# Kernel optimization log

Measured on AMD Instinct MI355X. Metric: run time of the kernel, lower is better.

## Reference

```python
import jax, jax.numpy as jnp
import numpy as np

N, A, C = 4096, 512, 100


def setup_inputs() -> dict:
    key = jax.random.key(0)
    k1, k2, k3 = jax.random.split(key, 3)
    features = jax.random.normal(k1, (N, A), dtype=jnp.float32)
    y_s = jax.random.normal(k2, (N, C), dtype=jnp.float32)
    labels = jax.random.randint(k3, (N,), 0, C, dtype=jnp.int64)
    CoVariance = jnp.zeros((C, A, A), dtype=jnp.float32)
    Ave = jnp.zeros((C, A), dtype=jnp.float32)
    Amount = jnp.zeros((C,), dtype=jnp.float32)
    return {"features": features, "y_s": y_s, "CoVariance": CoVariance,
            "Ave": Ave, "Amount": Amount, "labels": labels}


def reference(features, y_s, CoVariance, Ave, Amount, labels):
    n, a = features.shape
    c = Ave.shape[0]
    dt = features.dtype

    onehot = jax.nn.one_hot(labels, c, dtype=dt)            # [N, C]
    counts = onehot.sum(axis=0)                             # [C]
    counts_safe = jnp.where(counts == 0, 1.0, counts)       # Amount_CxA==0 -> 1

    # per-class mean: ave_CxA [C, A]
    sum_feats = onehot.T @ features                          # [C, A]
    ave_CxA = sum_feats / counts_safe[:, None]

    # centered features w.r.t. own-class mean; masked per-class copies
    centered = features - ave_CxA[labels]                    # [N, A]
    masked = onehot.T[:, :, None] * centered[None, :, :]     # [C, N, A]
    # per-class scatter of outer products (equals torch bmm over zero-padded rows)
    var_temp = jnp.einsum('cna,nb->cab', masked, centered) / counts_safe[:, None, None]

    # mixing weights; NaN (0/0) -> 0
    denom = counts + Amount                                  # [C]
    w = jnp.where(denom > 0, counts / denom, 0.0)            # [C]

    ave_old = jax.lax.stop_gradient(Ave)                     # .detach() in torch
    cov_old = jax.lax.stop_gradient(CoVariance)
    diff = ave_old - ave_CxA                                 # [C, A]
    additional_CV = (w * (1.0 - w))[:, None, None] * jnp.einsum('ca,cb->cab', diff, diff)

    new_cov = cov_old * (1.0 - w)[:, None, None] + var_temp * w[:, None, None] + additional_CV
    new_ave = ave_old * (1.0 - w)[:, None] + ave_CxA * w[:, None]
    new_amount = Amount + counts

    logp = jax.nn.log_softmax(y_s, axis=-1)                  # [N, C]
    loss = -jnp.mean(jnp.take_along_axis(logp, labels[:, None], axis=1))

    return loss, new_cov, new_ave, new_amount
```

## Files before the change

### kernel.cpp

```cpp
#include <hip/hip_runtime.h>


#define TM 128
#define KC 16
#define LSTR 132

__global__ void fused_prep(const int* __restrict__ labels, const float* __restrict__ Amount,
                           int* __restrict__ offsets, int* __restrict__ cursors,
                           float* __restrict__ w_arr, float* __restrict__ inv_cs,
                           float* __restrict__ amount_out, float* __restrict__ loss_acc,
                           int N, int C) {
    __shared__ int hist[1024];
    __shared__ int offs[1025];
    int tid = threadIdx.x;
    for (int c = tid; c < C; c += blockDim.x) hist[c] = 0;
    __syncthreads();
    for (int i = tid; i < N; i += blockDim.x) atomicAdd(&hist[labels[i]], 1);
    __syncthreads();
    if (tid == 0) {
        int o = 0;
        for (int c = 0; c < C; ++c) { offs[c] = o; o += hist[c]; }
        offs[C] = o;
    }
    __syncthreads();
    for (int c = tid; c < C; c += blockDim.x) {
        float cf = (float)hist[c];
        float cs = cf > 0.f ? cf : 1.f;
        inv_cs[c] = 1.f / cs;
        float am = Amount[c];
        float dn = cf + am;
        w_arr[c] = dn > 0.f ? cf / dn : 0.f;
        amount_out[c] = am + cf;
        offsets[c] = offs[c];
        cursors[c] = 0;
    }
    if (tid == 0) { offsets[C] = offs[C]; loss_acc[0] = 0.f; }
}

__global__ void scatter_kernel(const int* __restrict__ labels, const int* __restrict__ offsets,
                               int* __restrict__ cursors, int* __restrict__ idx_sorted, int N) {
    int n = blockIdx.x * blockDim.x + threadIdx.x;
    if (n < N) {
        int c = labels[n];
        int pos = atomicAdd(&cursors[c], 1);
        idx_sorted[offsets[c] + pos] = n;
    }
}

__global__ __launch_bounds__(128) void ave_kernel(
    const float* __restrict__ feats, const float* __restrict__ Ave_in,
    const int* __restrict__ idx_sorted, const int* __restrict__ offsets,
    const float* __restrict__ w_arr, const float* __restrict__ inv_cs,
    float* __restrict__ ave_new, float* __restrict__ ave_out, int A) {
    __shared__ int idxs[512];
    const int c = blockIdx.y;
    const int col = blockIdx.x * 128 + threadIdx.x;
    const int base = offsets[c];
    const int nc = offsets[c + 1] - base;
    float sum = 0.f;
    for (int i0 = 0; i0 < nc; i0 += 512) {
        int chunk = min(512, nc - i0);
        __syncthreads();
        for (int j = threadIdx.x; j < chunk; j += 128) idxs[j] = idx_sorted[base + i0 + j];
        __syncthreads();
        int j = 0;
        for (; j + 3 < chunk; j += 4) {
            int r0 = idxs[j], r1 = idxs[j + 1], r2 = idxs[j + 2], r3 = idxs[j + 3];
            float f0 = feats[(size_t)r0 * A + col];
            float f1 = feats[(size_t)r1 * A + col];
            float f2 = feats[(size_t)r2 * A + col];
            float f3 = feats[(size_t)r3 * A + col];
            sum += f0 + f1 + f2 + f3;
        }
        for (; j < chunk; ++j) sum += feats[(size_t)idxs[j] * A + col];
    }
    float av = sum * inv_cs[c];
    ave_new[(size_t)c * A + col] = av;
    float w = w_arr[c];
    ave_out[(size_t)c * A + col] = Ave_in[(size_t)c * A + col] * (1.f - w) + av * w;
}

__global__ __launch_bounds__(256) void cov_kernel(
    const float* __restrict__ feats, const float* __restrict__ cov_in,
    const float* __restrict__ ave_new, const float* __restrict__ Ave_in,
    const int* __restrict__ idx_sorted, const int* __restrict__ offsets,
    const float* __restrict__ w_arr, const float* __restrict__ inv_cs,
    float* __restrict__ cov_out, int A) {
    const int c  = blockIdx.z;
    const int a0 = blockIdx.y * TM;
    const int b0 = blockIdx.x * TM;
    const int tid = threadIdx.x;
    const int ty = tid >> 4, tx = tid & 15;

    __shared__ float Xa[KC][LSTR];
    __shared__ float Xb[KC][LSTR];
    __shared__ float aveA[TM], aveB[TM], dA[TM], dB[TM];

    if (tid < TM) {
        float av = ave_new[(size_t)c * A + a0 + tid];
        aveA[tid] = av;
        dA[tid] = Ave_in[(size_t)c * A + a0 + tid] - av;
    } else {
        int t = tid - TM;
        float bv = ave_new[(size_t)c * A + b0 + t];
        aveB[t] = bv;
        dB[t] = Ave_in[(size_t)c * A + b0 + t] - bv;
    }

    const float w   = w_arr[c];
    const float omw = 1.f - w;
    const float s   = inv_cs[c] * w;
    const float aw  = w * omw;
    const size_t cbase = (size_t)c * A * A;

    float acc[2][4][2][4] = {};

    if (s > 0.f) {
        if (omw != 0.f) {
            const float sc = omw / s;
            #pragma unroll
            for (int ri = 0; ri < 2; ++ri)
                #pragma unroll
                for (int i = 0; i < 4; ++i) {
                    const size_t rowo = cbase + (size_t)(a0 + ri * 64 + ty * 4 + i) * A + b0;
                    #pragma unroll
                    for (int ci = 0; ci < 2; ++ci) {
                        float4 co = *reinterpret_cast<const float4*>(&cov_in[rowo + ci * 64 + tx * 4]);
                        acc[ri][i][ci][0] = co.x * sc;
                        acc[ri][i][ci][1] = co.y * sc;
                        acc[ri][i][ci][2] = co.z * sc;
                        acc[ri][i][ci][3] = co.w * sc;
                    }
                }
        }

        const int base = offsets[c];
        const int nc = offsets[c + 1] - base;
        const int li = ty;
        const int cg = tx * 4;

        __syncthreads();

        for (int kk = 0; kk < nc; kk += KC) {
            const int kn = min(KC, nc - kk);
            float4 va0 = make_float4(0.f, 0.f, 0.f, 0.f), va1 = va0, vb0 = va0, vb1 = va0;
            if (li < kn) {
                int row = idx_sorted[base + kk + li];
                const float* fr = feats + (size_t)row * A;
                va0 = *reinterpret_cast<const float4*>(fr + a0 + cg);
                va1 = *reinterpret_cast<const float4*>(fr + a0 + cg + 64);
                vb0 = *reinterpret_cast<const float4*>(fr + b0 + cg);
                vb1 = *reinterpret_cast<const float4*>(fr + b0 + cg + 64);
                va0.x -= aveA[cg];      va0.y -= aveA[cg + 1];      va0.z -= aveA[cg + 2];      va0.w -= aveA[cg + 3];
                va1.x -= aveA[cg + 64]; va1.y -= aveA[cg + 65];     va1.z -= aveA[cg + 66];     va1.w -= aveA[cg + 67];
                vb0.x -= aveB[cg];      vb0.y -= aveB[cg + 1];      vb0.z -= aveB[cg + 2];      vb0.w -= aveB[cg + 3];
                vb1.x -= aveB[cg + 64]; vb1.y -= aveB[cg + 65];     vb1.z -= aveB[cg + 66];     vb1.w -= aveB[cg + 67];
            }
            __syncthreads();
            *reinterpret_cast<float4*>(&Xa[li][cg])      = va0;
            *reinterpret_cast<float4*>(&Xa[li][cg + 64]) = va1;
            *reinterpret_cast<float4*>(&Xb[li][cg])      = vb0;
            *reinterpret_cast<float4*>(&Xb[li][cg + 64]) = vb1;
            __syncthreads();

            #pragma unroll
            for (int k = 0; k < KC; ++k) {
                float4 a0v = *reinterpret_cast<const float4*>(&Xa[k][ty * 4]);
                float4 a1v = *reinterpret_cast<const float4*>(&Xa[k][64 + ty * 4]);
                float4 b0v = *reinterpret_cast<const float4*>(&Xb[k][tx * 4]);
                float4 b1v = *reinterpret_cast<const float4*>(&Xb[k][64 + tx * 4]);
                float af[2][4] = {{a0v.x, a0v.y, a0v.z, a0v.w}, {a1v.x, a1v.y, a1v.z, a1v.w}};
                float bf[2][4] = {{b0v.x, b0v.y, b0v.z, b0v.w}, {b1v.x, b1v.y, b1v.z, b1v.w}};
                #pragma unroll
                for (int ri = 0; ri < 2; ++ri)
                    #pragma unroll
                    for (int i = 0; i < 4; ++i)
                        #pragma unroll
                        for (int ci = 0; ci < 2; ++ci)
                            #pragma unroll
                            for (int j = 0; j < 4; ++j)
                                acc[ri][i][ci][j] += af[ri][i] * bf[ci][j];
            }
        }

        float db[2][4];
        #pragma unroll
        for (int ci = 0; ci < 2; ++ci)
            #pragma unroll
            for (int j = 0; j < 4; ++j) db[ci][j] = dB[ci * 64 + tx * 4 + j];

        #pragma unroll
        for (int ri = 0; ri < 2; ++ri)
            #pragma unroll
            for (int i = 0; i < 4; ++i) {
                float da = dA[ri * 64 + ty * 4 + i];
                const size_t rowo = cbase + (size_t)(a0 + ri * 64 + ty * 4 + i) * A + b0;
                #pragma unroll
                for (int ci = 0; ci < 2; ++ci) {
                    float4 res;
                    res.x = acc[ri][i][ci][0] * s + aw * da * db[ci][0];
                    res.y = acc[ri][i][ci][1] * s + aw * da * db[ci][1];
                    res.z = acc[ri][i][ci][2] * s + aw * da * db[ci][2];
                    res.w = acc[ri][i][ci][3] * s + aw * da * db[ci][3];
                    *reinterpret_cast<float4*>(&cov_out[rowo + ci * 64 + tx * 4]) = res;
                }
            }
    } else {
        #pragma unroll
        for (int ri = 0; ri < 2; ++ri)
            #pragma unroll
            for (int i = 0; i < 4; ++i) {
                const size_t rowo = cbase + (size_t)(a0 + ri * 64 + ty * 4 + i) * A + b0;
                #pragma unroll
                for (int ci = 0; ci < 2; ++ci) {
                    float4 co = *reinterpret_cast<const float4*>(&cov_in[rowo + ci * 64 + tx * 4]);
                    float4 res = make_float4(co.x * omw, co.y * omw, co.z * omw, co.w * omw);
                    *reinterpret_cast<float4*>(&cov_out[rowo + ci * 64 + tx * 4]) = res;
                }
            }
    }
}

__global__ __launch_bounds__(256) void loss_kernel(
    const float* __restrict__ y_s, const int* __restrict__ labels,
    float* __restrict__ loss_acc, int N, int C) {
    __shared__ float bsum[4];
    const int lane = threadIdx.x & 63;
    const int wv = threadIdx.x >> 6;
    const int gw = blockIdx.x * 4 + wv;
    const int nwaves = gridDim.x * 4;
    float wsum = 0.f;
    for (int r = gw; r < N; r += nwaves) {
        const float* row = y_s + (size_t)r * C;
        float m = -1e30f;
        for (int col = lane; col < C; col += 64) m = fmaxf(m, row[col]);
        #pragma unroll
        for (int off = 32; off > 0; off >>= 1) m = fmaxf(m, __shfl_xor(m, off));
        float se = 0.f;
        for (int col = lane; col < C; col += 64) se += __expf(row[col] - m);
        #pragma unroll
        for (int off = 32; off > 0; off >>= 1) se += __shfl_xor(se, off);
        if (lane == 0) wsum += -(row[labels[r]] - m - __logf(se));
    }
    if (lane == 0) bsum[wv] = wsum;
    __syncthreads();
    if (threadIdx.x == 0) {
        float t = bsum[0] + bsum[1] + bsum[2] + bsum[3];
        atomicAdd(loss_acc, t);
    }
}

__global__ void finalize_kernel(const float* __restrict__ loss_acc, float* __restrict__ out_loss,
                                float invN) {
    if (threadIdx.x == 0 && blockIdx.x == 0) out_loss[0] = loss_acc[0] * invN;
}

extern "C" void kernel_launch(void* const* d_in, const int* in_sizes, int n_in,
                              void* d_out, int out_size, void* d_ws, size_t ws_size,
                              hipStream_t stream) {
    const float* feats  = (const float*)d_in[0];
    const float* y_s    = (const float*)d_in[1];
    const float* cov_in = (const float*)d_in[2];
    const float* Ave_in = (const float*)d_in[3];
    const float* Amount = (const float*)d_in[4];
    const int*   labels = (const int*)d_in[5];

    const int C = in_sizes[4];
    const int N = in_sizes[5];
    const int A = in_sizes[3] / C;

    float* out      = (float*)d_out;
    float* out_loss = out;
    float* out_cov  = out + 1;
    float* out_ave  = out_cov + (size_t)C * A * A;
    float* out_amt  = out_ave + (size_t)C * A;

    char* w8 = (char*)d_ws;
    int* offsets    = (int*)w8;   w8 += (size_t)(C + 1) * sizeof(int);
    int* cursors    = (int*)w8;   w8 += (size_t)C * sizeof(int);
    int* idx_sorted = (int*)w8;   w8 += (size_t)N * sizeof(int);
    float* loss_acc = (float*)w8; w8 += sizeof(float);
    float* w_arr    = (float*)w8; w8 += (size_t)C * sizeof(float);
    float* inv_cs   = (float*)w8; w8 += (size_t)C * sizeof(float);
    float* ave_new  = (float*)w8; w8 += (size_t)C * A * sizeof(float);

    fused_prep<<<1, 1024, 0, stream>>>(labels, Amount, offsets, cursors, w_arr, inv_cs,
                                       out_amt, loss_acc, N, C);
    scatter_kernel<<<(N + 255) / 256, 256, 0, stream>>>(labels, offsets, cursors, idx_sorted, N);
    ave_kernel<<<dim3(A / 128, C), 128, 0, stream>>>(feats, Ave_in, idx_sorted, offsets,
                                                     w_arr, inv_cs, ave_new, out_ave, A);
    dim3 grid(A / TM, A / TM, C);
    cov_kernel<<<grid, 256, 0, stream>>>(feats, cov_in, ave_new, Ave_in, idx_sorted, offsets,
                                         w_arr, inv_cs, out_cov, A);
    loss_kernel<<<64, 256, 0, stream>>>(y_s, labels, loss_acc, N, C);
    finalize_kernel<<<1, 64, 0, stream>>>(loss_acc, out_loss, 1.f / (float)N);
}
```

Baseline: 263.6 us.

## Use bf16 MFMA for per-class covariance and fuse prep/scatter/finalize kernels

Moves the per-class covariance outer-product accumulation from FP32 FMA tiles to bf16 MFMA 16x16x32 instructions. Centered features are rounded to bf16 and staged transposed in LDS, with a K-chunk of 32. The scatter of sorted indices is folded into the single-block prep kernel using LDS cursors, and the loss finalize kernel is removed by pre-scaling the atomic adds. Together these cut FP32 ALU cost and launch overhead, but they reduce precision of the covariance and use scalar, less-coalesced global stores in the MFMA output layout.

After: 270.4 us. +2.6%, slower.

```diff
diff --git a/kernel.cpp b/kernel.cpp
--- a/kernel.cpp
+++ b/kernel.cpp
@@ -2,20 +2,30 @@
 
 
 #define TM 128
-#define KC 16
-#define LSTR 132
-
-__global__ void fused_prep(const int* __restrict__ labels, const float* __restrict__ Amount,
-                           int* __restrict__ offsets, int* __restrict__ cursors,
-                           float* __restrict__ w_arr, float* __restrict__ inv_cs,
-                           float* __restrict__ amount_out, float* __restrict__ loss_acc,
-                           int N, int C) {
+#define KC 32
+#define KCP 40
+
+typedef __attribute__((ext_vector_type(8))) short bf16x8;
+typedef __attribute__((ext_vector_type(4))) float f32x4;
+
+__device__ __forceinline__ unsigned short f2bf(float f) {
+    unsigned u = __float_as_uint(f);
+    u += 0x7fffu + ((u >> 16) & 1u);
+    return (unsigned short)(u >> 16);
+}
+
+__global__ __launch_bounds__(1024) void prep_kernel(
+    const int* __restrict__ labels, const float* __restrict__ Amount,
+    int* __restrict__ offsets, int* __restrict__ idx_sorted,
+    float* __restrict__ w_arr, float* __restrict__ inv_cs,
+    float* __restrict__ amount_out, float* __restrict__ out_loss0, int N, int C) {
     __shared__ int hist[1024];
     __shared__ int offs[1025];
-    int tid = threadIdx.x;
-    for (int c = tid; c < C; c += blockDim.x) hist[c] = 0;
-    __syncthreads();
-    for (int i = tid; i < N; i += blockDim.x) atomicAdd(&hist[labels[i]], 1);
+    __shared__ int cur[1024];
+    const int tid = threadIdx.x;
+    for (int c = tid; c < C; c += 1024) { hist[c] = 0; cur[c] = 0; }
+    __syncthreads();
+    for (int i = tid; i < N; i += 1024) atomicAdd(&hist[labels[i]], 1);
     __syncthreads();
     if (tid == 0) {
         int o = 0;
@@ -23,7 +33,7 @@
         offs[C] = o;
     }
     __syncthreads();
-    for (int c = tid; c < C; c += blockDim.x) {
+    for (int c = tid; c < C; c += 1024) {
         float cf = (float)hist[c];
         float cs = cf > 0.f ? cf : 1.f;
         inv_cs[c] = 1.f / cs;
@@ -32,18 +42,12 @@
         w_arr[c] = dn > 0.f ? cf / dn : 0.f;
         amount_out[c] = am + cf;
         offsets[c] = offs[c];
-        cursors[c] = 0;
-    }
-    if (tid == 0) { offsets[C] = offs[C]; loss_acc[0] = 0.f; }
-}
-
-__global__ void scatter_kernel(const int* __restrict__ labels, const int* __restrict__ offsets,
-                               int* __restrict__ cursors, int* __restrict__ idx_sorted, int N) {
-    int n = blockIdx.x * blockDim.x + threadIdx.x;
-    if (n < N) {
-        int c = labels[n];
-        int pos = atomicAdd(&cursors[c], 1);
-        idx_sorted[offsets[c] + pos] = n;
+    }
+    if (tid == 0) { offsets[C] = offs[C]; out_loss0[0] = 0.f; }
+    for (int i = tid; i < N; i += 1024) {
+        int c = labels[i];
+        int p = atomicAdd(&cur[c], 1);
+        idx_sorted[offs[c] + p] = i;
     }
 }
 
@@ -65,11 +69,10 @@
         __syncthreads();
         int j = 0;
         for (; j + 3 < chunk; j += 4) {
-            int r0 = idxs[j], r1 = idxs[j + 1], r2 = idxs[j + 2], r3 = idxs[j + 3];
-            float f0 = feats[(size_t)r0 * A + col];
-            float f1 = feats[(size_t)r1 * A + col];
-            float f2 = feats[(size_t)r2 * A + col];
-            float f3 = feats[(size_t)r3 * A + col];
+            float f0 = feats[(size_t)idxs[j] * A + col];
+            float f1 = feats[(size_t)idxs[j + 1] * A + col];
+            float f2 = feats[(size_t)idxs[j + 2] * A + col];
+            float f3 = feats[(size_t)idxs[j + 3] * A + col];
             sum += f0 + f1 + f2 + f3;
         }
         for (; j < chunk; ++j) sum += feats[(size_t)idxs[j] * A + col];
@@ -90,22 +93,10 @@
     const int a0 = blockIdx.y * TM;
     const int b0 = blockIdx.x * TM;
     const int tid = threadIdx.x;
-    const int ty = tid >> 4, tx = tid & 15;
-
-    __shared__ float Xa[KC][LSTR];
-    __shared__ float Xb[KC][LSTR];
-    __shared__ float aveA[TM], aveB[TM], dA[TM], dB[TM];
-
-    if (tid < TM) {
-        float av = ave_new[(size_t)c * A + a0 + tid];
-        aveA[tid] = av;
-        dA[tid] = Ave_in[(size_t)c * A + a0 + tid] - av;
-    } else {
-        int t = tid - TM;
-        float bv = ave_new[(size_t)c * A + b0 + t];
-        aveB[t] = bv;
-        dB[t] = Ave_in[(size_t)c * A + b0 + t] - bv;
-    }
+
+    __shared__ __align__(16) unsigned short XT[2][TM][KCP];
+    __shared__ float dA[TM], dB[TM];
+    __shared__ int idx_lds[KC];
 
     const float w   = w_arr[c];
     const float omw = 1.f - w;
@@ -113,117 +104,109 @@
     const float aw  = w * omw;
     const size_t cbase = (size_t)c * A * A;
 
-    float acc[2][4][2][4] = {};
-
     if (s > 0.f) {
+        const int side = tid >> 7;
+        const int col  = tid & 127;
+        const int gcol = (side ? b0 : a0) + col;
+        const float mean = ave_new[(size_t)c * A + gcol];
+        if (side == 0) dA[col] = Ave_in[(size_t)c * A + gcol] - mean;
+        else           dB[col] = Ave_in[(size_t)c * A + gcol] - mean;
+
+        const int wave = tid >> 6;
+        const int qm = wave >> 1, qn = wave & 1;
+        const int lane = tid & 63;
+        const int lq = lane >> 4, lr = lane & 15;
+
+        f32x4 acc[4][4];
         if (omw != 0.f) {
             const float sc = omw / s;
             #pragma unroll
-            for (int ri = 0; ri < 2; ++ri)
-                #pragma unroll
-                for (int i = 0; i < 4; ++i) {
-                    const size_t rowo = cbase + (size_t)(a0 + ri * 64 + ty * 4 + i) * A + b0;
+            for (int i = 0; i < 4; ++i)
+                #pragma unroll
+                for (int j = 0; j < 4; ++j) {
+                    const int n = qn * 64 + j * 16 + lr;
                     #pragma unroll
-                    for (int ci = 0; ci < 2; ++ci) {
-                        float4 co = *reinterpret_cast<const float4*>(&cov_in[rowo + ci * 64 + tx * 4]);
-                        acc[ri][i][ci][0] = co.x * sc;
-                        acc[ri][i][ci][1] = co.y * sc;
-                        acc[ri][i][ci][2] = co.z * sc;
-                        acc[ri][i][ci][3] = co.w * sc;
+                    for (int reg = 0; reg < 4; ++reg) {
+                        const int m = qm * 64 + i * 16 + lq * 4 + reg;
+                        acc[i][j][reg] = cov_in[cbase + (size_t)(a0 + m) * A + b0 + n] * sc;
                     }
                 }
+        } else {
+            #pragma unroll
+            for (int i = 0; i < 4; ++i)
+                #pragma unroll
+                for (int j = 0; j < 4; ++j)
+                    acc[i][j] = (f32x4){0.f, 0.f, 0.f, 0.f};
         }
 
         const int base = offsets[c];
         const int nc = offsets[c + 1] - base;
-        const int li = ty;
-        const int cg = tx * 4;
-
-        __syncthreads();
 
         for (int kk = 0; kk < nc; kk += KC) {
-            const int kn = min(KC, nc - kk);
-            float4 va0 = make_float4(0.f, 0.f, 0.f, 0.f), va1 = va0, vb0 = va0, vb1 = va0;
-            if (li < kn) {
-                int row = idx_sorted[base + kk + li];
-                const float* fr = feats + (size_t)row * A;
-                va0 = *reinterpret_cast<const float4*>(fr + a0 + cg);
-                va1 = *reinterpret_cast<const float4*>(fr + a0 + cg + 64);
-                vb0 = *reinterpret_cast<const float4*>(fr + b0 + cg);
-                vb1 = *reinterpret_cast<const float4*>(fr + b0 + cg + 64);
-                va0.x -= aveA[cg];      va0.y -= aveA[cg + 1];      va0.z -= aveA[cg + 2];      va0.w -= aveA[cg + 3];
-                va1.x -= aveA[cg + 64]; va1.y -= aveA[cg + 65];     va1.z -= aveA[cg + 66];     va1.w -= aveA[cg + 67];
-                vb0.x -= aveB[cg];      vb0.y -= aveB[cg + 1];      vb0.z -= aveB[cg + 2];      vb0.w -= aveB[cg + 3];
-                vb1.x -= aveB[cg + 64]; vb1.y -= aveB[cg + 65];     vb1.z -= aveB[cg + 66];     vb1.w -= aveB[cg + 67];
+            __syncthreads();
+            if (tid < KC) idx_lds[tid] = (kk + tid < nc) ? idx_sorted[base + kk + tid] : 0;
+            __syncthreads();
+            #pragma unroll
+            for (int mg = 0; mg < KC / 4; ++mg) {
+                unsigned short q0, q1, q2, q3;
+                {
+                    int m = mg * 4;
+                    float v0 = (kk + m + 0 < nc) ? feats[(size_t)idx_lds[m + 0] * A + gcol] - mean : 0.f;
+                    float v1 = (kk + m + 1 < nc) ? feats[(size_t)idx_lds[m + 1] * A + gcol] - mean : 0.f;
+                    float v2 = (kk + m + 2 < nc) ? feats[(size_t)idx_lds[m + 2] * A + gcol] - mean : 0.f;
+                    float v3 = (kk + m + 3 < nc) ? feats[(size_t)idx_lds[m + 3] * A + gcol] - mean : 0.f;
+                    q0 = f2bf(v0); q1 = f2bf(v1); q2 = f2bf(v2); q3 = f2bf(v3);
+                }
+                uint2 pk;
+                pk.x = (unsigned)q0 | ((unsigned)q1 << 16);
+                pk.y = (unsigned)q2 | ((unsigned)q3 << 16);
+                *reinterpret_cast<uint2*>(&XT[side][col][mg * 4]) = pk;
             }
             __syncthreads();
-            *reinterpret_cast<float4*>(&Xa[li][cg])      = va0;
-            *reinterpret_cast<float4*>(&Xa[li][cg + 64]) = va1;
-            *reinterpret_cast<float4*>(&Xb[li][cg])      = vb0;
-            *reinterpret_cast<float4*>(&Xb[li][cg + 64]) = vb1;
-            __syncthreads();
-
-            #pragma unroll
-            for (int k = 0; k < KC; ++k) {
-                float4 a0v = *reinterpret_cast<const float4*>(&Xa[k][ty * 4]);
-                float4 a1v = *reinterpret_cast<const float4*>(&Xa[k][64 + ty * 4]);
-                float4 b0v = *reinterpret_cast<const float4*>(&Xb[k][tx * 4]);
-                float4 b1v = *reinterpret_cast<const float4*>(&Xb[k][64 + tx * 4]);
-                float af[2][4] = {{a0v.x, a0v.y, a0v.z, a0v.w}, {a1v.x, a1v.y, a1v.z, a1v.w}};
-                float bf[2][4] = {{b0v.x, b0v.y, b0v.z, b0v.w}, {b1v.x, b1v.y, b1v.z, b1v.w}};
-                #pragma unroll
-                for (int ri = 0; ri < 2; ++ri)
-                    #pragma unroll
-                    for (int i = 0; i < 4; ++i)
-                        #pragma unroll
-                        for (int ci = 0; ci < 2; ++ci)
-                            #pragma unroll
-                            for (int j = 0; j < 4; ++j)
-                                acc[ri][i][ci][j] += af[ri][i] * bf[ci][j];
-            }
-        }
-
-        float db[2][4];
+            bf16x8 af[4], bfr[4];
+            #pragma unroll
+            for (int i = 0; i < 4; ++i)
+                af[i] = *reinterpret_cast<const bf16x8*>(&XT[0][qm * 64 + i * 16 + lr][lq * 8]);
+            #pragma unroll
+            for (int j = 0; j < 4; ++j)
+                bfr[j] = *reinterpret_cast<const bf16x8*>(&XT[1][qn * 64 + j * 16 + lr][lq * 8]);
+            #pragma unroll
+            for (int i = 0; i < 4; ++i)
+                #pragma unroll
+                for (int j = 0; j < 4; ++j)
+                    acc[i][j] = __builtin_amdgcn_mfma_f32_16x16x32_bf16(af[i], bfr[j], acc[i][j], 0, 0, 0);
+        }
+
         #pragma unroll
-        for (int ci = 0; ci < 2; ++ci)
-            #pragma unroll
-            for (int j = 0; j < 4; ++j) db[ci][j] = dB[ci * 64 + tx * 4 + j];
-
-        #pragma unroll
-        for (int ri = 0; ri < 2; ++ri)
-            #pragma unroll
-            for (int i = 0; i < 4; ++i) {
-                float da = dA[ri * 64 + ty * 4 + i];
-                const size_t rowo = cbase + (size_t)(a0 + ri * 64 + ty * 4 + i) * A + b0;
-                #pragma unroll
-                for (int ci = 0; ci < 2; ++ci) {
-                    float4 res;
-                    res.x = acc[ri][i][ci][0] * s + aw * da * db[ci][0];
-                    res.y = acc[ri][i][ci][1] * s + aw * da * db[ci][1];
-                    res.z = acc[ri][i][ci][2] * s + aw * da * db[ci][2];
-                    res.w = acc[ri][i][ci][3] * s + aw * da * db[ci][3];
-                    *reinterpret_cast<float4*>(&cov_out[rowo + ci * 64 + tx * 4]) = res;
+        for (int i = 0; i < 4; ++i) {
+            #pragma unroll
+            for (int reg = 0; reg < 4; ++reg) {
+                const int m = qm * 64 + i * 16 + lq * 4 + reg;
+                const float da = aw * dA[m];
+                float* rowp = cov_out + cbase + (size_t)(a0 + m) * A + b0;
+                #pragma unroll
+                for (int j = 0; j < 4; ++j) {
+                    const int n = qn * 64 + j * 16 + lr;
+                    rowp[n] = acc[i][j][reg] * s + da * dB[n];
                 }
             }
+        }
     } else {
-        #pragma unroll
-        for (int ri = 0; ri < 2; ++ri)
-            #pragma unroll
-            for (int i = 0; i < 4; ++i) {
-                const size_t rowo = cbase + (size_t)(a0 + ri * 64 + ty * 4 + i) * A + b0;
-                #pragma unroll
-                for (int ci = 0; ci < 2; ++ci) {
-                    float4 co = *reinterpret_cast<const float4*>(&cov_in[rowo + ci * 64 + tx * 4]);
-                    float4 res = make_float4(co.x * omw, co.y * omw, co.z * omw, co.w * omw);
-                    *reinterpret_cast<float4*>(&cov_out[rowo + ci * 64 + tx * 4]) = res;
-                }
-            }
+        const float sc = omw;
+        for (int t = tid; t < TM * TM / 4; t += 256) {
+            const int r = t >> 5;
+            const int c4 = (t & 31) * 4;
+            const size_t o = cbase + (size_t)(a0 + r) * A + b0 + c4;
+            float4 co = *reinterpret_cast<const float4*>(&cov_in[o]);
+            float4 res = make_float4(co.x * sc, co.y * sc, co.z * sc, co.w * sc);
+            *reinterpret_cast<float4*>(&cov_out[o]) = res;
+        }
     }
 }
 
 __global__ __launch_bounds__(256) void loss_kernel(
     const float* __restrict__ y_s, const int* __restrict__ labels,
-    float* __restrict__ loss_acc, int N, int C) {
+    float* __restrict__ out_loss0, int N, int C, float invN) {
     __shared__ float bsum[4];
     const int lane = threadIdx.x & 63;
     const int wv = threadIdx.x >> 6;
@@ -245,14 +228,9 @@
     if (lane == 0) bsum[wv] = wsum;
     __syncthreads();
     if (threadIdx.x == 0) {
-        float t = bsum[0] + bsum[1] + bsum[2] + bsum[3];
-        atomicAdd(loss_acc, t);
-    }
-}
-
-__global__ void finalize_kernel(const float* __restrict__ loss_acc, float* __restrict__ out_loss,
-                                float invN) {
-    if (threadIdx.x == 0 && blockIdx.x == 0) out_loss[0] = loss_acc[0] * invN;
+        float t = (bsum[0] + bsum[1] + bsum[2] + bsum[3]) * invN;
+        atomicAdd(out_loss0, t);
+    }
 }
 
 extern "C" void kernel_launch(void* const* d_in, const int* in_sizes, int n_in,
@@ -277,21 +255,17 @@
 
     char* w8 = (char*)d_ws;
     int* offsets    = (int*)w8;   w8 += (size_t)(C + 1) * sizeof(int);
-    int* cursors    = (int*)w8;   w8 += (size_t)C * sizeof(int);
     int* idx_sorted = (int*)w8;   w8 += (size_t)N * sizeof(int);
-    float* loss_acc = (float*)w8; w8 += sizeof(float);
     float* w_arr    = (float*)w8; w8 += (size_t)C * sizeof(float);
     float* inv_cs   = (float*)w8; w8 += (size_t)C * sizeof(float);
     float* ave_new  = (float*)w8; w8 += (size_t)C * A * sizeof(float);
 
-    fused_prep<<<1, 1024, 0, stream>>>(labels, Amount, offsets, cursors, w_arr, inv_cs,
-                                       out_amt, loss_acc, N, C);
-    scatter_kernel<<<(N + 255) / 256, 256, 0, stream>>>(labels, offsets, cursors, idx_sorted, N);
+    prep_kernel<<<1, 1024, 0, stream>>>(labels, Amount, offsets, idx_sorted,
+                                        w_arr, inv_cs, out_amt, out_loss, N, C);
     ave_kernel<<<dim3(A / 128, C), 128, 0, stream>>>(feats, Ave_in, idx_sorted, offsets,
                                                      w_arr, inv_cs, ave_new, out_ave, A);
     dim3 grid(A / TM, A / TM, C);
     cov_kernel<<<grid, 256, 0, stream>>>(feats, cov_in, ave_new, Ave_in, idx_sorted, offsets,
                                          w_arr, inv_cs, out_cov, A);
-    loss_kernel<<<64, 256, 0, stream>>>(y_s, labels, loss_acc, N, C);
-    finalize_kernel<<<1, 64, 0, stream>>>(loss_acc, out_loss, 1.f / (float)N);
-}
+    loss_kernel<<<64, 256, 0, stream>>>(y_s, labels, out_loss, N, C, 1.f / (float)N);
+}
```

## Fuse scatter into prep; fold mean and loss into covariance kernel

Applied to the files above, without the earlier changes.

Moves the label scatter into the single-block prep kernel using shared-memory cursors. The separate per-class mean kernel and the loss and finalize kernels are removed. Each covariance tile block now recomputes its own column means, and an extra z-slice of the grid computes the loss by atomically adding pre-scaled partial sums. This cuts the launch count from six to two and drops the ave_new round trip through memory, at the cost of every tile block re-reading the class rows to build its means, which is redundant work.

Result: slower. 344.0 us (+30.5%).

```diff
diff --git a/kernel.cpp b/kernel.cpp
--- a/kernel.cpp
+++ b/kernel.cpp
@@ -5,17 +5,18 @@
 #define KC 16
 #define LSTR 132
 
-__global__ void fused_prep(const int* __restrict__ labels, const float* __restrict__ Amount,
-                           int* __restrict__ offsets, int* __restrict__ cursors,
-                           float* __restrict__ w_arr, float* __restrict__ inv_cs,
-                           float* __restrict__ amount_out, float* __restrict__ loss_acc,
-                           int N, int C) {
+__global__ __launch_bounds__(1024) void prep_kernel(
+    const int* __restrict__ labels, const float* __restrict__ Amount,
+    int* __restrict__ offsets, int* __restrict__ idx_sorted,
+    float* __restrict__ w_arr, float* __restrict__ inv_cs,
+    float* __restrict__ amount_out, float* __restrict__ out_loss0, int N, int C) {
     __shared__ int hist[1024];
     __shared__ int offs[1025];
-    int tid = threadIdx.x;
-    for (int c = tid; c < C; c += blockDim.x) hist[c] = 0;
-    __syncthreads();
-    for (int i = tid; i < N; i += blockDim.x) atomicAdd(&hist[labels[i]], 1);
+    __shared__ int cur[1024];
+    const int tid = threadIdx.x;
+    for (int c = tid; c < C; c += 1024) { hist[c] = 0; cur[c] = 0; }
+    __syncthreads();
+    for (int i = tid; i < N; i += 1024) atomicAdd(&hist[labels[i]], 1);
     __syncthreads();
     if (tid == 0) {
         int o = 0;
@@ -23,7 +24,7 @@
         offs[C] = o;
     }
     __syncthreads();
-    for (int c = tid; c < C; c += blockDim.x) {
+    for (int c = tid; c < C; c += 1024) {
         float cf = (float)hist[c];
         float cs = cf > 0.f ? cf : 1.f;
         inv_cs[c] = 1.f / cs;
@@ -32,90 +33,94 @@
         w_arr[c] = dn > 0.f ? cf / dn : 0.f;
         amount_out[c] = am + cf;
         offsets[c] = offs[c];
-        cursors[c] = 0;
-    }
-    if (tid == 0) { offsets[C] = offs[C]; loss_acc[0] = 0.f; }
+    }
+    if (tid == 0) { offsets[C] = offs[C]; out_loss0[0] = 0.f; }
+    for (int i = tid; i < N; i += 1024) {
+        int c = labels[i];
+        int p = atomicAdd(&cur[c], 1);
+        idx_sorted[offs[c] + p] = i;
+    }
 }
 
-__global__ void scatter_kernel(const int* __restrict__ labels, const int* __restrict__ offsets,
-                               int* __restrict__ cursors, int* __restrict__ idx_sorted, int N) {
-    int n = blockIdx.x * blockDim.x + threadIdx.x;
-    if (n < N) {
-        int c = labels[n];
-        int pos = atomicAdd(&cursors[c], 1);
-        idx_sorted[offsets[c] + pos] = n;
-    }
-}
-
-__global__ __launch_bounds__(128) void ave_kernel(
-    const float* __restrict__ feats, const float* __restrict__ Ave_in,
-    const int* __restrict__ idx_sorted, const int* __restrict__ offsets,
-    const float* __restrict__ w_arr, const float* __restrict__ inv_cs,
-    float* __restrict__ ave_new, float* __restrict__ ave_out, int A) {
-    __shared__ int idxs[512];
-    const int c = blockIdx.y;
-    const int col = blockIdx.x * 128 + threadIdx.x;
-    const int base = offsets[c];
-    const int nc = offsets[c + 1] - base;
-    float sum = 0.f;
-    for (int i0 = 0; i0 < nc; i0 += 512) {
-        int chunk = min(512, nc - i0);
+__global__ __launch_bounds__(256) void fused_kernel(
+    const float* __restrict__ feats, const float* __restrict__ cov_in,
+    const float* __restrict__ Ave_in, const float* __restrict__ y_s,
+    const int* __restrict__ labels, const int* __restrict__ idx_sorted,
+    const int* __restrict__ offsets, const float* __restrict__ w_arr,
+    const float* __restrict__ inv_cs,
+    float* __restrict__ out_cov, float* __restrict__ out_ave,
+    float* __restrict__ out_loss0, int N, int C, int A, float invN) {
+
+    if ((int)blockIdx.z == C) {
+        __shared__ float bsum[4];
+        const int lane = threadIdx.x & 63;
+        const int wv = threadIdx.x >> 6;
+        const int gw = ((blockIdx.y * gridDim.x + blockIdx.x) << 2) + wv;
+        const int nwaves = gridDim.x * gridDim.y * 4;
+        float wsum = 0.f;
+        for (int r = gw; r < N; r += nwaves) {
+            const float* row = y_s + (size_t)r * C;
+            float m = -1e30f;
+            for (int col = lane; col < C; col += 64) m = fmaxf(m, row[col]);
+            #pragma unroll
+            for (int off = 32; off > 0; off >>= 1) m = fmaxf(m, __shfl_xor(m, off));
+            float se = 0.f;
+            for (int col = lane; col < C; col += 64) se += __expf(row[col] - m);
+            #pragma unroll
+            for (int off = 32; off > 0; off >>= 1) se += __shfl_xor(se, off);
+            if (lane == 0) wsum += -(row[labels[r]] - m - __logf(se));
+        }
+        if (lane == 0) bsum[wv] = wsum;
         __syncthreads();
-        for (int j = threadIdx.x; j < chunk; j += 128) idxs[j] = idx_sorted[base + i0 + j];
-        __syncthreads();
-        int j = 0;
-        for (; j + 3 < chunk; j += 4) {
-            int r0 = idxs[j], r1 = idxs[j + 1], r2 = idxs[j + 2], r3 = idxs[j + 3];
-            float f0 = feats[(size_t)r0 * A + col];
-            float f1 = feats[(size_t)r1 * A + col];
-            float f2 = feats[(size_t)r2 * A + col];
-            float f3 = feats[(size_t)r3 * A + col];
-            sum += f0 + f1 + f2 + f3;
-        }
-        for (; j < chunk; ++j) sum += feats[(size_t)idxs[j] * A + col];
-    }
-    float av = sum * inv_cs[c];
-    ave_new[(size_t)c * A + col] = av;
-    float w = w_arr[c];
-    ave_out[(size_t)c * A + col] = Ave_in[(size_t)c * A + col] * (1.f - w) + av * w;
-}
-
-__global__ __launch_bounds__(256) void cov_kernel(
-    const float* __restrict__ feats, const float* __restrict__ cov_in,
-    const float* __restrict__ ave_new, const float* __restrict__ Ave_in,
-    const int* __restrict__ idx_sorted, const int* __restrict__ offsets,
-    const float* __restrict__ w_arr, const float* __restrict__ inv_cs,
-    float* __restrict__ cov_out, int A) {
+        if (threadIdx.x == 0)
+            atomicAdd(out_loss0, (bsum[0] + bsum[1] + bsum[2] + bsum[3]) * invN);
+        return;
+    }
+
     const int c  = blockIdx.z;
     const int a0 = blockIdx.y * TM;
     const int b0 = blockIdx.x * TM;
     const int tid = threadIdx.x;
-    const int ty = tid >> 4, tx = tid & 15;
 
     __shared__ float Xa[KC][LSTR];
     __shared__ float Xb[KC][LSTR];
     __shared__ float aveA[TM], aveB[TM], dA[TM], dB[TM];
 
-    if (tid < TM) {
-        float av = ave_new[(size_t)c * A + a0 + tid];
-        aveA[tid] = av;
-        dA[tid] = Ave_in[(size_t)c * A + a0 + tid] - av;
-    } else {
-        int t = tid - TM;
-        float bv = ave_new[(size_t)c * A + b0 + t];
-        aveB[t] = bv;
-        dB[t] = Ave_in[(size_t)c * A + b0 + t] - bv;
-    }
-
+    const int base = offsets[c];
+    const int nc = offsets[c + 1] - base;
     const float w   = w_arr[c];
     const float omw = 1.f - w;
     const float s   = inv_cs[c] * w;
     const float aw  = w * omw;
     const size_t cbase = (size_t)c * A * A;
 
-    float acc[2][4][2][4] = {};
+    const int side = tid >> 7;
+    const int col  = tid & 127;
+    const int gcol = (side ? b0 : a0) + col;
+    float sum = 0.f;
+    {
+        int j = 0;
+        for (; j + 3 < nc; j += 4) {
+            int r0 = idx_sorted[base + j];
+            int r1 = idx_sorted[base + j + 1];
+            int r2 = idx_sorted[base + j + 2];
+            int r3 = idx_sorted[base + j + 3];
+            sum += feats[(size_t)r0 * A + gcol] + feats[(size_t)r1 * A + gcol]
+                 + feats[(size_t)r2 * A + gcol] + feats[(size_t)r3 * A + gcol];
+        }
+        for (; j < nc; ++j) sum += feats[(size_t)idx_sorted[base + j] * A + gcol];
+    }
+    const float mean = sum * inv_cs[c];
+    if (side == 0) { aveA[col] = mean; dA[col] = Ave_in[(size_t)c * A + gcol] - mean; }
+    else           { aveB[col] = mean; dB[col] = Ave_in[(size_t)c * A + gcol] - mean; }
+    if (blockIdx.x == 0 && side == 0)
+        out_ave[(size_t)c * A + gcol] = Ave_in[(size_t)c * A + gcol] * omw + mean * w;
+    __syncthreads();
+
+    const int ty = tid >> 4, tx = tid & 15;
 
     if (s > 0.f) {
+        float acc[2][4][2][4] = {};
         if (omw != 0.f) {
             const float sc = omw / s;
             #pragma unroll
@@ -134,12 +139,8 @@
                 }
         }
 
-        const int base = offsets[c];
-        const int nc = offsets[c + 1] - base;
         const int li = ty;
         const int cg = tx * 4;
-
-        __syncthreads();
 
         for (int kk = 0; kk < nc; kk += KC) {
             const int kn = min(KC, nc - kk);
@@ -151,10 +152,10 @@
                 va1 = *reinterpret_cast<const float4*>(fr + a0 + cg + 64);
                 vb0 = *reinterpret_cast<const float4*>(fr + b0 + cg);
                 vb1 = *reinterpret_cast<const float4*>(fr + b0 + cg + 64);
-                va0.x -= aveA[cg];      va0.y -= aveA[cg + 1];      va0.z -= aveA[cg + 2];      va0.w -= aveA[cg + 3];
-                va1.x -= aveA[cg + 64]; va1.y -= aveA[cg + 65];     va1.z -= aveA[cg + 66];     va1.w -= aveA[cg + 67];
-                vb0.x -= aveB[cg];      vb0.y -= aveB[cg + 1];      vb0.z -= aveB[cg + 2];      vb0.w -= aveB[cg + 3];
-                vb1.x -= aveB[cg + 64]; vb1.y -= aveB[cg + 65];     vb1.z -= aveB[cg + 66];     vb1.w -= aveB[cg + 67];
+                va0.x -= aveA[cg];      va0.y -= aveA[cg + 1];  va0.z -= aveA[cg + 2];  va0.w -= aveA[cg + 3];
+                va1.x -= aveA[cg + 64]; va1.y -= aveA[cg + 65]; va1.z -= aveA[cg + 66]; va1.w -= aveA[cg + 67];
+                vb0.x -= aveB[cg];      vb0.y -= aveB[cg + 1];  vb0.z -= aveB[cg + 2];  vb0.w -= aveB[cg + 3];
+                vb1.x -= aveB[cg + 64]; vb1.y -= aveB[cg + 65]; vb1.z -= aveB[cg + 66]; vb1.w -= aveB[cg + 67];
             }
             __syncthreads();
             *reinterpret_cast<float4*>(&Xa[li][cg])      = va0;
@@ -193,66 +194,28 @@
         for (int ri = 0; ri < 2; ++ri)
             #pragma unroll
             for (int i = 0; i < 4; ++i) {
-                float da = dA[ri * 64 + ty * 4 + i];
+                float da = aw * dA[ri * 64 + ty * 4 + i];
                 const size_t rowo = cbase + (size_t)(a0 + ri * 64 + ty * 4 + i) * A + b0;
                 #pragma unroll
                 for (int ci = 0; ci < 2; ++ci) {
                     float4 res;
-                    res.x = acc[ri][i][ci][0] * s + aw * da * db[ci][0];
-                    res.y = acc[ri][i][ci][1] * s + aw * da * db[ci][1];
-                    res.z = acc[ri][i][ci][2] * s + aw * da * db[ci][2];
-                    res.w = acc[ri][i][ci][3] * s + aw * da * db[ci][3];
-                    *reinterpret_cast<float4*>(&cov_out[rowo + ci * 64 + tx * 4]) = res;
+                    res.x = acc[ri][i][ci][0] * s + da * db[ci][0];
+                    res.y = acc[ri][i][ci][1] * s + da * db[ci][1];
+                    res.z = acc[ri][i][ci][2] * s + da * db[ci][2];
+                    res.w = acc[ri][i][ci][3] * s + da * db[ci][3];
+                    *reinterpret_cast<float4*>(&out_cov[rowo + ci * 64 + tx * 4]) = res;
                 }
             }
     } else {
-        #pragma unroll
-        for (int ri = 0; ri < 2; ++ri)
-            #pragma unroll
-            for (int i = 0; i < 4; ++i) {
-                const size_t rowo = cbase + (size_t)(a0 + ri * 64 + ty * 4 + i) * A + b0;
-                #pragma unroll
-                for (int ci = 0; ci < 2; ++ci) {
-                    float4 co = *reinterpret_cast<const float4*>(&cov_in[rowo + ci * 64 + tx * 4]);
-                    float4 res = make_float4(co.x * omw, co.y * omw, co.z * omw, co.w * omw);
-                    *reinterpret_cast<float4*>(&cov_out[rowo + ci * 64 + tx * 4]) = res;
-                }
-            }
-    }
-}
-
-__global__ __launch_bounds__(256) void loss_kernel(
-    const float* __restrict__ y_s, const int* __restrict__ labels,
-    float* __restrict__ loss_acc, int N, int C) {
-    __shared__ float bsum[4];
-    const int lane = threadIdx.x & 63;
-    const int wv = threadIdx.x >> 6;
-    const int gw = blockIdx.x * 4 + wv;
-    const int nwaves = gridDim.x * 4;
-    float wsum = 0.f;
-    for (int r = gw; r < N; r += nwaves) {
-        const float* row = y_s + (size_t)r * C;
-        float m = -1e30f;
-        for (int col = lane; col < C; col += 64) m = fmaxf(m, row[col]);
-        #pragma unroll
-        for (int off = 32; off > 0; off >>= 1) m = fmaxf(m, __shfl_xor(m, off));
-        float se = 0.f;
-        for (int col = lane; col < C; col += 64) se += __expf(row[col] - m);
-        #pragma unroll
-        for (int off = 32; off > 0; off >>= 1) se += __shfl_xor(se, off);
-        if (lane == 0) wsum += -(row[labels[r]] - m - __logf(se));
-    }
-    if (lane == 0) bsum[wv] = wsum;
-    __syncthreads();
-    if (threadIdx.x == 0) {
-        float t = bsum[0] + bsum[1] + bsum[2] + bsum[3];
-        atomicAdd(loss_acc, t);
-    }
-}
-
-__global__ void finalize_kernel(const float* __restrict__ loss_acc, float* __restrict__ out_loss,
-                                float invN) {
-    if (threadIdx.x == 0 && blockIdx.x == 0) out_loss[0] = loss_acc[0] * invN;
+        for (int t = tid; t < TM * TM / 4; t += 256) {
+            const int r = t >> 5;
+            const int c4 = (t & 31) * 4;
+            const size_t o = cbase + (size_t)(a0 + r) * A + b0 + c4;
+            float4 co = *reinterpret_cast<const float4*>(&cov_in[o]);
+            *reinterpret_cast<float4*>(&out_cov[o]) =
+                make_float4(co.x * omw, co.y * omw, co.z * omw, co.w * omw);
+        }
+    }
 }
 
 extern "C" void kernel_launch(void* const* d_in, const int* in_sizes, int n_in,
@@ -277,21 +240,15 @@
 
     char* w8 = (char*)d_ws;
     int* offsets    = (int*)w8;   w8 += (size_t)(C + 1) * sizeof(int);
-    int* cursors    = (int*)w8;   w8 += (size_t)C * sizeof(int);
     int* idx_sorted = (int*)w8;   w8 += (size_t)N * sizeof(int);
-    float* loss_acc = (float*)w8; w8 += sizeof(float);
     float* w_arr    = (float*)w8; w8 += (size_t)C * sizeof(float);
     float* inv_cs   = (float*)w8; w8 += (size_t)C * sizeof(float);
-    float* ave_new  = (float*)w8; w8 += (size_t)C * A * sizeof(float);
-
-    fused_prep<<<1, 1024, 0, stream>>>(labels, Amount, offsets, cursors, w_arr, inv_cs,
-                                       out_amt, loss_acc, N, C);
-    scatter_kernel<<<(N + 255) / 256, 256, 0, stream>>>(labels, offsets, cursors, idx_sorted, N);
-    ave_kernel<<<dim3(A / 128, C), 128, 0, stream>>>(feats, Ave_in, idx_sorted, offsets,
-                                                     w_arr, inv_cs, ave_new, out_ave, A);
-    dim3 grid(A / TM, A / TM, C);
-    cov_kernel<<<grid, 256, 0, stream>>>(feats, cov_in, ave_new, Ave_in, idx_sorted, offsets,
-                                         w_arr, inv_cs, out_cov, A);
-    loss_kernel<<<64, 256, 0, stream>>>(y_s, labels, loss_acc, N, C);
-    finalize_kernel<<<1, 64, 0, stream>>>(loss_acc, out_loss, 1.f / (float)N);
+
+    prep_kernel<<<1, 1024, 0, stream>>>(labels, Amount, offsets, idx_sorted,
+                                        w_arr, inv_cs, out_amt, out_loss, N, C);
+    dim3 grid(A / TM, A / TM, C + 1);
+    fused_kernel<<<grid, 256, 0, stream>>>(feats, cov_in, Ave_in, y_s, labels,
+                                           idx_sorted, offsets, w_arr, inv_cs,
+                                           out_cov, out_ave, out_loss,
+                                           N, C, A, 1.f / (float)N);
 }
```
